# Kernel optimization log

Measured on AMD Instinct MI355X. Metric: run time of the kernel, lower is better.

The kernel has to match this reference:

```python
import jax, jax.numpy as jnp
import numpy as np

B, S, D_IN, D_OUT, H = 2, 2048, 1024, 1024, 16
HD = D_OUT // H  # head dim = 64


def setup_inputs() -> dict:
    key = jax.random.key(0)
    ks = jax.random.split(key, 9)
    s_in = 1.0 / np.sqrt(D_IN)
    s_out = 1.0 / np.sqrt(D_OUT)
    return {
        "X": jax.random.normal(ks[0], (B, S, D_IN), dtype=jnp.float32),
        "Wq": jax.random.uniform(ks[1], (D_OUT, D_IN), jnp.float32, -s_in, s_in),
        "bq": jax.random.uniform(ks[2], (D_OUT,), jnp.float32, -s_in, s_in),
        "Wk": jax.random.uniform(ks[3], (D_OUT, D_IN), jnp.float32, -s_in, s_in),
        "bk": jax.random.uniform(ks[4], (D_OUT,), jnp.float32, -s_in, s_in),
        "Wv": jax.random.uniform(ks[5], (D_OUT, D_IN), jnp.float32, -s_in, s_in),
        "bv": jax.random.uniform(ks[6], (D_OUT,), jnp.float32, -s_in, s_in),
        "Wo": jax.random.uniform(ks[7], (D_OUT, D_OUT), jnp.float32, -s_out, s_out),
        "bo": jax.random.uniform(ks[8], (D_OUT,), jnp.float32, -s_out, s_out),
    }


def reference(X, Wq, bq, Wk, bk, Wv, bv, Wo, bo):
    scale = jnp.asarray(HD ** 0.5, X.dtype)  # self.dim = sqrt(head_dim)
    q = X @ Wq.T + bq  # [B,S,D_OUT]
    k = X @ Wk.T + bk
    v = X @ Wv.T + bv
    # split heads: b s (h d) -> b h s d
    q = q.reshape(B, S, H, HD).transpose(0, 2, 1, 3)
    k = k.reshape(B, S, H, HD).transpose(0, 2, 1, 3)
    v = v.reshape(B, S, H, HD).transpose(0, 2, 1, 3)
    scores = jnp.einsum('bhsd,bhtd->bhst', q, k) / scale  # [B,H,S,S]
    causal = jnp.triu(jnp.ones((S, S), dtype=bool), k=1)
    scores = jnp.where(causal, -jnp.inf, scores)
    weights = jax.nn.softmax(scores, axis=-1)
    out = jnp.einsum('bhst,bhtd->bhsd', weights, v)  # [B,H,S,HD]
    out = out.transpose(0, 2, 1, 3).reshape(B, S, D_OUT)  # b h s d -> b s (h d)
    return out @ Wo.T + bo
```

## Files before the change

### kernel.cpp

```cpp
#include <hip/hip_runtime.h>
#include <hip/hip_bf16.h>

typedef __bf16 bf16_t;
typedef __bf16 bf16x8 __attribute__((ext_vector_type(8)));
typedef float  f32x4  __attribute__((ext_vector_type(4)));
typedef unsigned short ushort_t;

#define MFMA16(a, b, c) __builtin_amdgcn_mfma_f32_16x16x32_bf16((a), (b), (c), 0, 0, 0)
#define GLDS16(g, l) __builtin_amdgcn_global_load_lds( \
    (const __attribute__((address_space(1))) unsigned int*)(g), \
    (__attribute__((address_space(3))) unsigned int*)(l), 16, 0, 0)


__global__ __launch_bounds__(64) void sniff_kernel(const ushort_t* __restrict__ x,
                                                   int* __restrict__ flag)
{
    const int t = threadIdx.x;
    const ushort_t u = x[2 * t];
    const int e = (u >> 7) & 0xFF;
    const unsigned long long m = __ballot(e >= 0xA0);
    if (t == 0) *flag = (m != 0ull) ? 1 : 0;
}

__global__ __launch_bounds__(256) void cvt_all(
    const void* __restrict__ X,  const void* __restrict__ W0, const void* __restrict__ W1,
    const void* __restrict__ W2, const void* __restrict__ W3,
    bf16_t* __restrict__ Xb, bf16_t* __restrict__ Wb, const int* __restrict__ flag)
{
    const long long i = (long long)(blockIdx.x * 256 + threadIdx.x) * 8;
    const void* src;
    bf16_t* dst;
    long long off;
    if (i < 4194304) { src = X; dst = Xb; off = i; }
    else {
        const int w = (int)((i - 4194304) >> 20);
        off = (i - 4194304) & 1048575;
        src = (w == 0) ? W0 : (w == 1) ? W1 : (w == 2) ? W2 : W3;
        dst = Wb + (size_t)w * 1048576;
    }
    if (*flag) {
        const float* s = (const float*)src + off;
        const float4 a = *(const float4*)(s);
        const float4 b = *(const float4*)(s + 4);
        bf16x8 o;
        o[0] = (bf16_t)a.x; o[1] = (bf16_t)a.y; o[2] = (bf16_t)a.z; o[3] = (bf16_t)a.w;
        o[4] = (bf16_t)b.x; o[5] = (bf16_t)b.y; o[6] = (bf16_t)b.z; o[7] = (bf16_t)b.w;
        *(bf16x8*)(dst + off) = o;
    } else {
        *(bf16x8*)(dst + off) = *(const bf16x8*)((const bf16_t*)src + off);
    }
}

__global__ __launch_bounds__(256) void cvt_bias(const void* __restrict__ b0, const void* __restrict__ b1,
                                                const void* __restrict__ b2, const void* __restrict__ b3,
                                                float* __restrict__ dst, const int* __restrict__ flag)
{
    const int t = blockIdx.x * 256 + threadIdx.x;
    if (*flag) {
        dst[t]        = ((const float*)b0)[t];
        dst[1024 + t] = ((const float*)b1)[t];
        dst[2048 + t] = ((const float*)b2)[t];
        dst[3072 + t] = ((const float*)b3)[t];
    } else {
        dst[t]        = (float)((const bf16_t*)b0)[t];
        dst[1024 + t] = (float)((const bf16_t*)b1)[t];
        dst[2048 + t] = (float)((const bf16_t*)b2)[t];
        dst[3072 + t] = (float)((const bf16_t*)b3)[t];
    }
}

__global__ __launch_bounds__(256) void gemm_nt(
    const bf16_t* __restrict__ A,
    const bf16_t* __restrict__ W0, const bf16_t* __restrict__ W1, const bf16_t* __restrict__ W2,
    const float* __restrict__ b0, const float* __restrict__ b1, const float* __restrict__ b2,
    void* __restrict__ C, int ldc, const int* __restrict__ flag, int is_out)
{
    __shared__ bf16_t Ash[128 * 64];
    __shared__ bf16_t Bsh[128 * 64];

    const int f32out = is_out ? *flag : 0;

    const int tid  = threadIdx.x;
    const int wid  = tid >> 6;
    const int lane = tid & 63;
    const int g    = lane >> 4;
    const int c    = lane & 15;

    const int m0  = blockIdx.x * 128;
    const int n0  = blockIdx.y * 128;
    const int mat = n0 >> 10;
    const bf16_t* W  = (mat == 0) ? W0 : (mat == 1) ? W1 : W2;
    const float*  bs = (mat == 0) ? b0 : (mat == 1) ? b1 : b2;
    const int nw = n0 & 1023;

    const int srow = lane >> 3;
    const int sblk = (lane & 7) ^ srow;
    const bf16_t* Ag = A + (size_t)(m0 + wid * 32 + srow) * 1024 + sblk * 8;
    const bf16_t* Wg = W + (size_t)(nw + wid * 32 + srow) * 1024 + sblk * 8;
    bf16_t* Asb = &Ash[wid * 32 * 64];
    bf16_t* Bsb = &Bsh[wid * 32 * 64];

    const int waveM = (wid >> 1) * 64;
    const int waveN = (wid & 1) * 64;

    f32x4 acc[4][4] = {};

    for (int k0 = 0; k0 < 1024; k0 += 64) {
        #pragma unroll
        for (int q = 0; q < 4; ++q) {
            GLDS16(Ag + (size_t)q * 8 * 1024 + k0, Asb + q * 8 * 64);
            GLDS16(Wg + (size_t)q * 8 * 1024 + k0, Bsb + q * 8 * 64);
        }
        __syncthreads();

        #pragma unroll
        for (int kb = 0; kb < 2; ++kb) {
            bf16x8 af[4], bfr[4];
            #pragma unroll
            for (int i = 0; i < 4; ++i) {
                const int row = waveM + i * 16 + c;
                af[i] = *(const bf16x8*)(&Ash[row * 64 + ((((kb << 2) | g) ^ (c & 7)) << 3)]);
            }
            #pragma unroll
            for (int j = 0; j < 4; ++j) {
                const int row = waveN + j * 16 + c;
                bfr[j] = *(const bf16x8*)(&Bsh[row * 64 + ((((kb << 2) | g) ^ (c & 7)) << 3)]);
            }
            #pragma unroll
            for (int i = 0; i < 4; ++i)
                #pragma unroll
                for (int j = 0; j < 4; ++j)
                    acc[i][j] = MFMA16(af[i], bfr[j], acc[i][j]);
        }
        __syncthreads();
    }

    #pragma unroll
    for (int j = 0; j < 4; ++j) {
        const int col = n0 + waveN + j * 16 + c;
        const float bv = bs[col & 1023];
        #pragma unroll
        for (int i = 0; i < 4; ++i) {
            const int row = m0 + waveM + i * 16 + g * 4;
            #pragma unroll
            for (int r = 0; r < 4; ++r) {
                const float val = acc[i][j][r] + bv;
                const size_t idx = (size_t)(row + r) * ldc + col;
                if (f32out) ((float*)C)[idx] = val;
                else        ((bf16_t*)C)[idx] = (bf16_t)val;
            }
        }
    }
}

__global__ __launch_bounds__(256) void transpose_v(
    const bf16_t* __restrict__ QKV, bf16_t* __restrict__ Vt)
{
    __shared__ ushort_t T[64][72];
    const int tid = threadIdx.x;
    const int r   = tid >> 2;
    const int c0  = (tid & 3) * 16;
    const int bh  = blockIdx.y;
    const int b   = bh >> 4, h = bh & 15;
    const int s0  = blockIdx.x * 64;

    const ushort_t* src = (const ushort_t*)QKV +
        (size_t)(b * 2048 + s0 + r) * 3072 + 2048 + h * 64 + c0;
    ushort_t v[16];
    *(uint4*)(&v[0]) = *(const uint4*)(src);
    *(uint4*)(&v[8]) = *(const uint4*)(src + 8);
    #pragma unroll
    for (int i = 0; i < 16; ++i) T[c0 + i][r] = v[i];
    __syncthreads();
    ushort_t* dst = (ushort_t*)Vt + ((size_t)bh * 64 + r) * 2048 + s0 + c0;
    *(uint4*)(dst)     = *(const uint4*)(&T[r][c0]);
    *(uint4*)(dst + 8) = *(const uint4*)(&T[r][c0 + 8]);
}

__global__ __launch_bounds__(256) void attn_kernel(
    const bf16_t* __restrict__ QKV, const bf16_t* __restrict__ Vt,
    bf16_t* __restrict__ O)
{
    __shared__ bf16_t Ksh[64][72];
    __shared__ bf16_t Vsh[64][72];
    __shared__ bf16_t Psh[4][32][72];

    const int tid  = threadIdx.x;
    const int wid  = tid >> 6;
    const int lane = tid & 63;
    const int g    = lane >> 4;
    const int c    = lane & 15;

    const int bh = blockIdx.y;
    const int b  = bh >> 4, h = bh & 15;
    const int qt = (bh < 16) ? blockIdx.x : (15 - blockIdx.x);
    const int q0 = qt * 128;
    const int nt = 2 * qt + 2;

    bf16x8 aq[2][2];
    #pragma unroll
    for (int qf = 0; qf < 2; ++qf) {
        const bf16_t* qp = QKV + (size_t)(b * 2048 + q0 + wid * 32 + qf * 16 + c) * 3072 + h * 64;
        #pragma unroll
        for (int kb = 0; kb < 2; ++kb) {
            bf16x8 t = *(const bf16x8*)(qp + kb * 32 + g * 8);
            #pragma unroll
            for (int j = 0; j < 8; ++j) t[j] = (bf16_t)((float)t[j] * 0.125f);
            aq[qf][kb] = t;
        }
    }

    float li[2][4] = {};
    f32x4 o[2][4]  = {};

    const int sr  = tid >> 2;
    const int sc0 = (tid & 3) * 16;
    const bf16_t* Kg = QKV + (size_t)(b * 2048 + sr) * 3072 + 1024 + h * 64 + sc0;
    const bf16_t* Vg = Vt + ((size_t)bh * 64 + sr) * 2048 + sc0;

    uint4 kr0 = *(const uint4*)(Kg);
    uint4 kr1 = *(const uint4*)(Kg + 8);
    uint4 vr0 = *(const uint4*)(Vg);
    uint4 vr1 = *(const uint4*)(Vg + 8);

    for (int jt = 0; jt < nt; ++jt) {
        *(uint4*)(&Ksh[sr][sc0])     = kr0;
        *(uint4*)(&Ksh[sr][sc0 + 8]) = kr1;
        *(uint4*)(&Vsh[sr][sc0])     = vr0;
        *(uint4*)(&Vsh[sr][sc0 + 8]) = vr1;
        __syncthreads();

        if (jt + 1 < nt) {
            const size_t ko = (size_t)(jt + 1) * 64 * 3072;
            kr0 = *(const uint4*)(Kg + ko);
            kr1 = *(const uint4*)(Kg + ko + 8);
            vr0 = *(const uint4*)(Vg + (jt + 1) * 64);
            vr1 = *(const uint4*)(Vg + (jt + 1) * 64 + 8);
        }

        f32x4 s[2][4] = {};
        #pragma unroll
        for (int n = 0; n < 4; ++n)
            #pragma unroll
            for (int kb = 0; kb < 2; ++kb) {
                const bf16x8 kf = *(const bf16x8*)(&Ksh[n * 16 + c][kb * 32 + g * 8]);
                s[0][n] = MFMA16(aq[0][kb], kf, s[0][n]);
                s[1][n] = MFMA16(aq[1][kb], kf, s[1][n]);
            }

        if (jt >= nt - 2) {
            const int j0 = jt * 64;
            #pragma unroll
            for (int qf = 0; qf < 2; ++qf) {
                const int qrow = q0 + wid * 32 + qf * 16 + g * 4;
                #pragma unroll
                for (int n = 0; n < 4; ++n)
                    #pragma unroll
                    for (int r = 0; r < 4; ++r)
                        if (j0 + n * 16 + c > qrow + r) s[qf][n][r] = -1e30f;
            }
        }

        #pragma unroll
        for (int qf = 0; qf < 2; ++qf)
            #pragma unroll
            for (int n = 0; n < 4; ++n)
                #pragma unroll
                for (int r = 0; r < 4; ++r) {
                    const float p = __expf(s[qf][n][r]);
                    li[qf][r] += p;
                    Psh[wid][qf * 16 + g * 4 + r][n * 16 + c] = (bf16_t)p;
                }
        __builtin_amdgcn_wave_barrier();

        #pragma unroll
        for (int kb = 0; kb < 2; ++kb) {
            const bf16x8 ap0 = *(const bf16x8*)(&Psh[wid][c][kb * 32 + g * 8]);
            const bf16x8 ap1 = *(const bf16x8*)(&Psh[wid][16 + c][kb * 32 + g * 8]);
            #pragma unroll
            for (int d = 0; d < 4; ++d) {
                const bf16x8 vf = *(const bf16x8*)(&Vsh[d * 16 + c][kb * 32 + g * 8]);
                o[0][d] = MFMA16(ap0, vf, o[0][d]);
                o[1][d] = MFMA16(ap1, vf, o[1][d]);
            }
        }
        __syncthreads();
    }

    #pragma unroll
    for (int off = 1; off < 16; off <<= 1)
        #pragma unroll
        for (int qf = 0; qf < 2; ++qf)
            #pragma unroll
            for (int r = 0; r < 4; ++r)
                li[qf][r] += __shfl_xor(li[qf][r], off, 64);

    #pragma unroll
    for (int qf = 0; qf < 2; ++qf) {
        const int orow = b * 2048 + q0 + wid * 32 + qf * 16 + g * 4;
        #pragma unroll
        for (int r = 0; r < 4; ++r) {
            const float inv = 1.0f / li[qf][r];
            #pragma unroll
            for (int d = 0; d < 4; ++d)
                O[(size_t)(orow + r) * 1024 + h * 64 + d * 16 + c] = (bf16_t)(o[qf][d][r] * inv);
        }
    }
}

extern "C" void kernel_launch(void* const* d_in, const int* in_sizes, int n_in,
                              void* d_out, int out_size, void* d_ws, size_t ws_size,
                              hipStream_t stream)
{
    const void* X  = d_in[0];
    const void* Wq = d_in[1];  const void* bq = d_in[2];
    const void* Wk = d_in[3];  const void* bk = d_in[4];
    const void* Wv = d_in[5];  const void* bv = d_in[6];
    const void* Wo = d_in[7];  const void* bo = d_in[8];

    int*    flag  = (int*)d_ws;
    float*  biasF = (float*)((char*)d_ws + 16);
    bf16_t* Xb    = (bf16_t*)((char*)d_ws + 16 + 16384);
    bf16_t* Wb    = Xb  + (size_t)4096 * 1024;
    bf16_t* QKV   = Wb  + (size_t)4 * 1024 * 1024;
    bf16_t* Vt    = QKV + (size_t)4096 * 3072;
    bf16_t* Ao    = Vt  + (size_t)4096 * 1024;

    const size_t MW = (size_t)1024 * 1024;

    sniff_kernel<<<1, 64, 0, stream>>>((const ushort_t*)X, flag);
    cvt_all<<<4096, 256, 0, stream>>>(X, Wq, Wk, Wv, Wo, Xb, Wb, flag);
    cvt_bias<<<4, 256, 0, stream>>>(bq, bk, bv, bo, biasF, flag);

    gemm_nt<<<dim3(32, 24), 256, 0, stream>>>(
        Xb, Wb, Wb + MW, Wb + 2 * MW,
        biasF, biasF + 1024, biasF + 2048, QKV, 3072, flag, 0);
    transpose_v<<<dim3(32, 32), 256, 0, stream>>>(QKV, Vt);
    attn_kernel<<<dim3(16, 32), 256, 0, stream>>>(QKV, Vt, Ao);
    gemm_nt<<<dim3(32, 8), 256, 0, stream>>>(
        Ao, Wb + 3 * MW, Wb + 3 * MW, Wb + 3 * MW,
        biasF + 3072, biasF + 3072, biasF + 3072, d_out, 1024, flag, 1);
}
```

Baseline: 221.3 us.

## Double-buffer LDS tiles in projection GEMM with K=32 steps and manual waitcnt

Restructures the NT GEMM main loop to use two LDS buffers of K=32 each, prefetching the next tile via global_load_lds while computing on the current one, with explicit vmcnt/lgkmcnt waits and raw barriers. It is meant to hide global-to-LDS load latency that the single-buffered loop exposed at every iteration. It halves the K per barrier, which doubles the number of synchronisations, and adds a new swizzle. It also relies on hand-encoded waitcnt immediates being correct for this target.

```diff
diff --git a/kernel.cpp b/kernel.cpp
--- a/kernel.cpp
+++ b/kernel.cpp
@@ -10,6 +10,10 @@
 #define GLDS16(g, l) __builtin_amdgcn_global_load_lds( \
     (const __attribute__((address_space(1))) unsigned int*)(g), \
     (__attribute__((address_space(3))) unsigned int*)(l), 16, 0, 0)
+
+#define WAITCNT_VM4   0x0F74
+#define WAITCNT_VM0   0x0F70
+#define WAITCNT_LGKM0 0xC07F
 
 
 __global__ __launch_bounds__(64) void sniff_kernel(const ushort_t* __restrict__ x,
@@ -75,8 +79,8 @@
     const float* __restrict__ b0, const float* __restrict__ b1, const float* __restrict__ b2,
     void* __restrict__ C, int ldc, const int* __restrict__ flag, int is_out)
 {
-    __shared__ bf16_t Ash[128 * 64];
-    __shared__ bf16_t Bsh[128 * 64];
+    __shared__ bf16_t Ash[2][128 * 32];
+    __shared__ bf16_t Bsh[2][128 * 32];
 
     const int f32out = is_out ? *flag : 0;
 
@@ -93,46 +97,78 @@
     const float*  bs = (mat == 0) ? b0 : (mat == 1) ? b1 : b2;
     const int nw = n0 & 1023;
 
-    const int srow = lane >> 3;
-    const int sblk = (lane & 7) ^ srow;
+    const int srow = lane >> 2;
+    const int sblk = (lane & 3) ^ ((lane >> 3) & 3);
     const bf16_t* Ag = A + (size_t)(m0 + wid * 32 + srow) * 1024 + sblk * 8;
     const bf16_t* Wg = W + (size_t)(nw + wid * 32 + srow) * 1024 + sblk * 8;
-    bf16_t* Asb = &Ash[wid * 32 * 64];
-    bf16_t* Bsb = &Bsh[wid * 32 * 64];
 
     const int waveM = (wid >> 1) * 64;
     const int waveN = (wid & 1) * 64;
 
     f32x4 acc[4][4] = {};
 
-    for (int k0 = 0; k0 < 1024; k0 += 64) {
-        #pragma unroll
-        for (int q = 0; q < 4; ++q) {
-            GLDS16(Ag + (size_t)q * 8 * 1024 + k0, Asb + q * 8 * 64);
-            GLDS16(Wg + (size_t)q * 8 * 1024 + k0, Bsb + q * 8 * 64);
-        }
-        __syncthreads();
-
-        #pragma unroll
-        for (int kb = 0; kb < 2; ++kb) {
-            bf16x8 af[4], bfr[4];
-            #pragma unroll
-            for (int i = 0; i < 4; ++i) {
-                const int row = waveM + i * 16 + c;
-                af[i] = *(const bf16x8*)(&Ash[row * 64 + ((((kb << 2) | g) ^ (c & 7)) << 3)]);
-            }
-            #pragma unroll
-            for (int j = 0; j < 4; ++j) {
-                const int row = waveN + j * 16 + c;
-                bfr[j] = *(const bf16x8*)(&Bsh[row * 64 + ((((kb << 2) | g) ^ (c & 7)) << 3)]);
-            }
-            #pragma unroll
-            for (int i = 0; i < 4; ++i)
-                #pragma unroll
-                for (int j = 0; j < 4; ++j)
-                    acc[i][j] = MFMA16(af[i], bfr[j], acc[i][j]);
-        }
-        __syncthreads();
+    const int fblk = (g ^ ((c >> 1) & 3)) * 8;
+
+    {
+        bf16_t* As = &Ash[0][(wid * 32) * 32];
+        bf16_t* Bs = &Bsh[0][(wid * 32) * 32];
+        GLDS16(Ag, As);
+        GLDS16(Ag + (size_t)16 * 1024, As + 16 * 32);
+        GLDS16(Wg, Bs);
+        GLDS16(Wg + (size_t)16 * 1024, Bs + 16 * 32);
+    }
+
+    #pragma unroll 4
+    for (int k = 0; k < 31; ++k) {
+        const int cur = k & 1;
+        const int nxt = cur ^ 1;
+        const int k0  = (k + 1) * 32;
+        {
+            bf16_t* As = &Ash[nxt][(wid * 32) * 32];
+            bf16_t* Bs = &Bsh[nxt][(wid * 32) * 32];
+            GLDS16(Ag + k0, As);
+            GLDS16(Ag + (size_t)16 * 1024 + k0, As + 16 * 32);
+            GLDS16(Wg + k0, Bs);
+            GLDS16(Wg + (size_t)16 * 1024 + k0, Bs + 16 * 32);
+        }
+        __builtin_amdgcn_s_waitcnt(WAITCNT_VM4);
+        __builtin_amdgcn_s_barrier();
+        asm volatile("" ::: "memory");
+
+        bf16x8 af[4], bfr[4];
+        #pragma unroll
+        for (int i = 0; i < 4; ++i)
+            af[i] = *(const bf16x8*)(&Ash[cur][(waveM + i * 16 + c) * 32 + fblk]);
+        #pragma unroll
+        for (int j = 0; j < 4; ++j)
+            bfr[j] = *(const bf16x8*)(&Bsh[cur][(waveN + j * 16 + c) * 32 + fblk]);
+        #pragma unroll
+        for (int i = 0; i < 4; ++i)
+            #pragma unroll
+            for (int j = 0; j < 4; ++j)
+                acc[i][j] = MFMA16(af[i], bfr[j], acc[i][j]);
+
+        asm volatile("" ::: "memory");
+        __builtin_amdgcn_s_waitcnt(WAITCNT_LGKM0);
+        __builtin_amdgcn_s_barrier();
+    }
+
+    __builtin_amdgcn_s_waitcnt(WAITCNT_VM0);
+    __builtin_amdgcn_s_barrier();
+    asm volatile("" ::: "memory");
+    {
+        bf16x8 af[4], bfr[4];
+        #pragma unroll
+        for (int i = 0; i < 4; ++i)
+            af[i] = *(const bf16x8*)(&Ash[1][(waveM + i * 16 + c) * 32 + fblk]);
+        #pragma unroll
+        for (int j = 0; j < 4; ++j)
+            bfr[j] = *(const bf16x8*)(&Bsh[1][(waveN + j * 16 + c) * 32 + fblk]);
+        #pragma unroll
+        for (int i = 0; i < 4; ++i)
+            #pragma unroll
+            for (int j = 0; j < 4; ++j)
+                acc[i][j] = MFMA16(af[i], bfr[j], acc[i][j]);
     }
 
     #pragma unroll
```

Result: no change. 221.6 us (+0.1%).

## Triple-buffer GEMM K loop, add M=64 output GEMM, widen attention KV tiles

Applied to the files above, without the earlier changes.

The GEMM now uses a three-stage LDS ring with BK=32, issuing global-to-LDS loads two steps ahead and waiting on vmcnt so copies overlap MFMA work. It is templated on M tile, and the output projection uses a 64-row tile to launch twice as many blocks. The attention kernel loads 128-key K/V tiles per iteration, halving the number of block-wide syncs and load rounds, but it uses more LDS and registers. The hand-written waitcnt encodings are a correctness risk if the load counts are wrong.

```diff
diff --git a/kernel.cpp b/kernel.cpp
--- a/kernel.cpp
+++ b/kernel.cpp
@@ -10,6 +10,9 @@
 #define GLDS16(g, l) __builtin_amdgcn_global_load_lds( \
     (const __attribute__((address_space(1))) unsigned int*)(g), \
     (__attribute__((address_space(3))) unsigned int*)(l), 16, 0, 0)
+
+#define WAITCNT_VM(n)  (0x0F70 | (n))
+#define WAITCNT_LGKM0  0xC07F
 
 
 __global__ __launch_bounds__(64) void sniff_kernel(const ushort_t* __restrict__ x,
@@ -69,14 +72,17 @@
     }
 }
 
+template<int TM>
 __global__ __launch_bounds__(256) void gemm_nt(
     const bf16_t* __restrict__ A,
     const bf16_t* __restrict__ W0, const bf16_t* __restrict__ W1, const bf16_t* __restrict__ W2,
     const float* __restrict__ b0, const float* __restrict__ b1, const float* __restrict__ b2,
     void* __restrict__ C, int ldc, const int* __restrict__ flag, int is_out)
 {
-    __shared__ bf16_t Ash[128 * 64];
-    __shared__ bf16_t Bsh[128 * 64];
+    constexpr int MI = TM / 32;
+    constexpr int G  = (TM == 128) ? 4 : 3;
+    __shared__ bf16_t Ash[3][TM * 32];
+    __shared__ bf16_t Bsh[3][128 * 32];
 
     const int f32out = is_out ? *flag : 0;
 
@@ -86,53 +92,67 @@
     const int g    = lane >> 4;
     const int c    = lane & 15;
 
-    const int m0  = blockIdx.x * 128;
+    const int m0  = blockIdx.x * TM;
     const int n0  = blockIdx.y * 128;
     const int mat = n0 >> 10;
     const bf16_t* W  = (mat == 0) ? W0 : (mat == 1) ? W1 : W2;
     const float*  bs = (mat == 0) ? b0 : (mat == 1) ? b1 : b2;
     const int nw = n0 & 1023;
 
-    const int srow = lane >> 3;
-    const int sblk = (lane & 7) ^ srow;
-    const bf16_t* Ag = A + (size_t)(m0 + wid * 32 + srow) * 1024 + sblk * 8;
+    const int srow = lane >> 2;
+    const int sblk = (lane & 3) ^ ((lane >> 3) & 3);
+    const bf16_t* Ag = A + (size_t)(m0 + wid * (TM / 4) + srow) * 1024 + sblk * 8;
     const bf16_t* Wg = W + (size_t)(nw + wid * 32 + srow) * 1024 + sblk * 8;
-    bf16_t* Asb = &Ash[wid * 32 * 64];
-    bf16_t* Bsb = &Bsh[wid * 32 * 64];
-
-    const int waveM = (wid >> 1) * 64;
+
+    const int waveM = (wid >> 1) * (TM / 2);
     const int waveN = (wid & 1) * 64;
 
-    f32x4 acc[4][4] = {};
-
-    for (int k0 = 0; k0 < 1024; k0 += 64) {
-        #pragma unroll
-        for (int q = 0; q < 4; ++q) {
-            GLDS16(Ag + (size_t)q * 8 * 1024 + k0, Asb + q * 8 * 64);
-            GLDS16(Wg + (size_t)q * 8 * 1024 + k0, Bsb + q * 8 * 64);
-        }
-        __syncthreads();
-
-        #pragma unroll
-        for (int kb = 0; kb < 2; ++kb) {
-            bf16x8 af[4], bfr[4];
-            #pragma unroll
-            for (int i = 0; i < 4; ++i) {
-                const int row = waveM + i * 16 + c;
-                af[i] = *(const bf16x8*)(&Ash[row * 64 + ((((kb << 2) | g) ^ (c & 7)) << 3)]);
-            }
-            #pragma unroll
-            for (int j = 0; j < 4; ++j) {
-                const int row = waveN + j * 16 + c;
-                bfr[j] = *(const bf16x8*)(&Bsh[row * 64 + ((((kb << 2) | g) ^ (c & 7)) << 3)]);
-            }
-            #pragma unroll
-            for (int i = 0; i < 4; ++i)
-                #pragma unroll
-                for (int j = 0; j < 4; ++j)
-                    acc[i][j] = MFMA16(af[i], bfr[j], acc[i][j]);
-        }
-        __syncthreads();
+    f32x4 acc[MI][4] = {};
+    const int fblk = (g ^ ((c >> 1) & 3)) * 8;
+
+    auto stage = [&](int t, int buf) {
+        const int k0 = t * 32;
+        bf16_t* As = &Ash[buf][(wid * (TM / 4)) * 32];
+        bf16_t* Bs = &Bsh[buf][(wid * 32) * 32];
+        GLDS16(Ag + k0, As);
+        if (TM == 128) GLDS16(Ag + (size_t)16 * 1024 + k0, As + 16 * 32);
+        GLDS16(Wg + k0, Bs);
+        GLDS16(Wg + (size_t)16 * 1024 + k0, Bs + 16 * 32);
+    };
+
+    stage(0, 0);
+    stage(1, 1);
+
+    #pragma unroll 3
+    for (int k = 0; k < 32; ++k) {
+        if (k < 30) {
+            stage(k + 2, (k + 2) % 3);
+            __builtin_amdgcn_s_waitcnt(WAITCNT_VM(2 * G));
+        } else if (k == 30) {
+            __builtin_amdgcn_s_waitcnt(WAITCNT_VM(G));
+        } else {
+            __builtin_amdgcn_s_waitcnt(WAITCNT_VM(0));
+        }
+        __builtin_amdgcn_s_barrier();
+        asm volatile("" ::: "memory");
+
+        const int cur = k % 3;
+        bf16x8 af[MI], bfr[4];
+        #pragma unroll
+        for (int i = 0; i < MI; ++i)
+            af[i] = *(const bf16x8*)(&Ash[cur][(waveM + i * 16 + c) * 32 + fblk]);
+        #pragma unroll
+        for (int j = 0; j < 4; ++j)
+            bfr[j] = *(const bf16x8*)(&Bsh[cur][(waveN + j * 16 + c) * 32 + fblk]);
+        #pragma unroll
+        for (int i = 0; i < MI; ++i)
+            #pragma unroll
+            for (int j = 0; j < 4; ++j)
+                acc[i][j] = MFMA16(af[i], bfr[j], acc[i][j]);
+
+        asm volatile("" ::: "memory");
+        __builtin_amdgcn_s_waitcnt(WAITCNT_LGKM0);
+        __builtin_amdgcn_s_barrier();
     }
 
     #pragma unroll
@@ -140,7 +160,7 @@
         const int col = n0 + waveN + j * 16 + c;
         const float bv = bs[col & 1023];
         #pragma unroll
-        for (int i = 0; i < 4; ++i) {
+        for (int i = 0; i < MI; ++i) {
             const int row = m0 + waveM + i * 16 + g * 4;
             #pragma unroll
             for (int r = 0; r < 4; ++r) {
@@ -181,8 +201,8 @@
     const bf16_t* __restrict__ QKV, const bf16_t* __restrict__ Vt,
     bf16_t* __restrict__ O)
 {
-    __shared__ bf16_t Ksh[64][72];
-    __shared__ bf16_t Vsh[64][72];
+    __shared__ bf16_t Ksh[128][72];
+    __shared__ bf16_t Vsh[64][136];
     __shared__ bf16_t Psh[4][32][72];
 
     const int tid  = threadIdx.x;
@@ -195,7 +215,7 @@
     const int b  = bh >> 4, h = bh & 15;
     const int qt = (bh < 16) ? blockIdx.x : (15 - blockIdx.x);
     const int q0 = qt * 128;
-    const int nt = 2 * qt + 2;
+    const int nt = qt + 1;
 
     bf16x8 aq[2][2];
     #pragma unroll
@@ -213,76 +233,80 @@
     float li[2][4] = {};
     f32x4 o[2][4]  = {};
 
-    const int sr  = tid >> 2;
-    const int sc0 = (tid & 3) * 16;
-    const bf16_t* Kg = QKV + (size_t)(b * 2048 + sr) * 3072 + 1024 + h * 64 + sc0;
-    const bf16_t* Vg = Vt + ((size_t)bh * 64 + sr) * 2048 + sc0;
-
-    uint4 kr0 = *(const uint4*)(Kg);
-    uint4 kr1 = *(const uint4*)(Kg + 8);
-    uint4 vr0 = *(const uint4*)(Vg);
-    uint4 vr1 = *(const uint4*)(Vg + 8);
+    const int ksr = tid >> 1;
+    const int kc0 = (tid & 1) * 32;
+    const int vsr = tid >> 2;
+    const int vc0 = (tid & 3) * 32;
+    const bf16_t* Kg = QKV + (size_t)(b * 2048 + ksr) * 3072 + 1024 + h * 64 + kc0;
+    const bf16_t* Vg = Vt + ((size_t)bh * 64 + vsr) * 2048 + vc0;
+
+    uint4 kr[4], vr[4];
+    #pragma unroll
+    for (int u = 0; u < 4; ++u) {
+        kr[u] = *(const uint4*)(Kg + u * 8);
+        vr[u] = *(const uint4*)(Vg + u * 8);
+    }
 
     for (int jt = 0; jt < nt; ++jt) {
-        *(uint4*)(&Ksh[sr][sc0])     = kr0;
-        *(uint4*)(&Ksh[sr][sc0 + 8]) = kr1;
-        *(uint4*)(&Vsh[sr][sc0])     = vr0;
-        *(uint4*)(&Vsh[sr][sc0 + 8]) = vr1;
+        #pragma unroll
+        for (int u = 0; u < 4; ++u) {
+            *(uint4*)(&Ksh[ksr][kc0 + u * 8]) = kr[u];
+            *(uint4*)(&Vsh[vsr][vc0 + u * 8]) = vr[u];
+        }
         __syncthreads();
 
         if (jt + 1 < nt) {
-            const size_t ko = (size_t)(jt + 1) * 64 * 3072;
-            kr0 = *(const uint4*)(Kg + ko);
-            kr1 = *(const uint4*)(Kg + ko + 8);
-            vr0 = *(const uint4*)(Vg + (jt + 1) * 64);
-            vr1 = *(const uint4*)(Vg + (jt + 1) * 64 + 8);
-        }
-
-        f32x4 s[2][4] = {};
-        #pragma unroll
-        for (int n = 0; n < 4; ++n)
-            #pragma unroll
-            for (int kb = 0; kb < 2; ++kb) {
-                const bf16x8 kf = *(const bf16x8*)(&Ksh[n * 16 + c][kb * 32 + g * 8]);
-                s[0][n] = MFMA16(aq[0][kb], kf, s[0][n]);
-                s[1][n] = MFMA16(aq[1][kb], kf, s[1][n]);
+            const size_t ko = (size_t)(jt + 1) * 128 * 3072;
+            const int    vo = (jt + 1) * 128;
+            #pragma unroll
+            for (int u = 0; u < 4; ++u) {
+                kr[u] = *(const uint4*)(Kg + ko + u * 8);
+                vr[u] = *(const uint4*)(Vg + vo + u * 8);
             }
-
-        if (jt >= nt - 2) {
-            const int j0 = jt * 64;
+        }
+
+        const bool last = (jt == nt - 1);
+        #pragma unroll
+        for (int half = 0; half < 2; ++half) {
             #pragma unroll
             for (int qf = 0; qf < 2; ++qf) {
-                const int qrow = q0 + wid * 32 + qf * 16 + g * 4;
+                f32x4 s[4] = {};
                 #pragma unroll
                 for (int n = 0; n < 4; ++n)
                     #pragma unroll
-                    for (int r = 0; r < 4; ++r)
-                        if (j0 + n * 16 + c > qrow + r) s[qf][n][r] = -1e30f;
+                    for (int kb = 0; kb < 2; ++kb) {
+                        const bf16x8 kf =
+                            *(const bf16x8*)(&Ksh[half * 64 + n * 16 + c][kb * 32 + g * 8]);
+                        s[n] = MFMA16(aq[qf][kb], kf, s[n]);
+                    }
+                const int qrow = q0 + wid * 32 + qf * 16 + g * 4;
+                const int jb   = jt * 128 + half * 64;
+                #pragma unroll
+                for (int n = 0; n < 4; ++n)
+                    #pragma unroll
+                    for (int r = 0; r < 4; ++r) {
+                        float v = s[n][r];
+                        if (last && (jb + n * 16 + c > qrow + r)) v = -1e30f;
+                        const float p = __expf(v);
+                        li[qf][r] += p;
+                        Psh[wid][qf * 16 + g * 4 + r][n * 16 + c] = (bf16_t)p;
+                    }
             }
-        }
-
-        #pragma unroll
-        for (int qf = 0; qf < 2; ++qf)
-            #pragma unroll
-            for (int n = 0; n < 4; ++n)
+            __builtin_amdgcn_wave_barrier();
+
+            #pragma unroll
+            for (int kb = 0; kb < 2; ++kb) {
+                const bf16x8 ap0 = *(const bf16x8*)(&Psh[wid][c][kb * 32 + g * 8]);
+                const bf16x8 ap1 = *(const bf16x8*)(&Psh[wid][16 + c][kb * 32 + g * 8]);
                 #pragma unroll
-                for (int r = 0; r < 4; ++r) {
-                    const float p = __expf(s[qf][n][r]);
-                    li[qf][r] += p;
-                    Psh[wid][qf * 16 + g * 4 + r][n * 16 + c] = (bf16_t)p;
+                for (int d = 0; d < 4; ++d) {
+                    const bf16x8 vf =
+                        *(const bf16x8*)(&Vsh[d * 16 + c][half * 64 + kb * 32 + g * 8]);
+                    o[0][d] = MFMA16(ap0, vf, o[0][d]);
+                    o[1][d] = MFMA16(ap1, vf, o[1][d]);
                 }
-        __builtin_amdgcn_wave_barrier();
-
-        #pragma unroll
-        for (int kb = 0; kb < 2; ++kb) {
-            const bf16x8 ap0 = *(const bf16x8*)(&Psh[wid][c][kb * 32 + g * 8]);
-            const bf16x8 ap1 = *(const bf16x8*)(&Psh[wid][16 + c][kb * 32 + g * 8]);
-            #pragma unroll
-            for (int d = 0; d < 4; ++d) {
-                const bf16x8 vf = *(const bf16x8*)(&Vsh[d * 16 + c][kb * 32 + g * 8]);
-                o[0][d] = MFMA16(ap0, vf, o[0][d]);
-                o[1][d] = MFMA16(ap1, vf, o[1][d]);
             }
+            __builtin_amdgcn_wave_barrier();
         }
         __syncthreads();
     }
@@ -332,12 +356,12 @@
     cvt_all<<<4096, 256, 0, stream>>>(X, Wq, Wk, Wv, Wo, Xb, Wb, flag);
     cvt_bias<<<4, 256, 0, stream>>>(bq, bk, bv, bo, biasF, flag);
 
-    gemm_nt<<<dim3(32, 24), 256, 0, stream>>>(
+    gemm_nt<128><<<dim3(32, 24), 256, 0, stream>>>(
         Xb, Wb, Wb + MW, Wb + 2 * MW,
         biasF, biasF + 1024, biasF + 2048, QKV, 3072, flag, 0);
     transpose_v<<<dim3(32, 32), 256, 0, stream>>>(QKV, Vt);
     attn_kernel<<<dim3(16, 32), 256, 0, stream>>>(QKV, Vt, Ao);
-    gemm_nt<<<dim3(32, 8), 256, 0, stream>>>(
+    gemm_nt<64><<<dim3(64, 8), 256, 0, stream>>>(
         Ao, Wb + 3 * MW, Wb + 3 * MW, Wb + 3 * MW,
         biasF + 3072, biasF + 3072, biasF + 3072, d_out, 1024, flag, 1);
 }
```

After: 259.9 us. 17.5% more time.
